# Kernel optimization log

Hardware: AMD Instinct MI355X
Metric: run time of the kernel (lower is better)

The kernel has to match this reference:

```python
import jax, jax.numpy as jnp
import numpy as np

N, T, IN, H, OUT, E = 50000, 12, 2, 128, 12, 800000


def setup_inputs() -> dict:
    key = jax.random.key(0)
    ks = jax.random.split(key, 20)
    s_in = 1.0 / np.sqrt(H)

    def w(k, shape):
        return jax.random.uniform(k, shape, jnp.float32, -s_in, s_in)

    return {
        "x": jax.random.normal(ks[0], (N, T, IN), jnp.float32),
        "edge_index": jax.random.randint(ks[1], (2, E), 0, N, dtype=jnp.int32),
        # LSTM layer 0 (input_dim -> H), gate order i,f,g,o as in PyTorch
        "Wih0": w(ks[2], (4 * H, IN)), "Whh0": w(ks[3], (4 * H, H)),
        "bih0": w(ks[4], (4 * H,)), "bhh0": w(ks[5], (4 * H,)),
        # LSTM layer 1 (H -> H)
        "Wih1": w(ks[6], (4 * H, H)), "Whh1": w(ks[7], (4 * H, H)),
        "bih1": w(ks[8], (4 * H,)), "bhh1": w(ks[9], (4 * H,)),
        # GCN layers
        "W0": w(ks[10], (H, H)), "b0": w(ks[11], (H,)),
        "W1": w(ks[12], (H, H)), "b1": w(ks[13], (H,)),
        "W2": w(ks[14], (H, OUT)), "b2": w(ks[15], (OUT,)),
    }


def _lstm_layer(seq, Wih, Whh, bih, bhh):
    # seq: [T, N, D] -> outputs [T, N, H]
    n = seq.shape[1]
    h0 = jnp.zeros((n, H), seq.dtype)
    c0 = jnp.zeros((n, H), seq.dtype)
    b = bih + bhh

    def step(carry, xt):
        h, c = carry
        z = xt @ Wih.T + h @ Whh.T + b
        i, f, g, o = jnp.split(z, 4, axis=-1)
        c = jax.nn.sigmoid(f) * c + jax.nn.sigmoid(i) * jnp.tanh(g)
        h = jax.nn.sigmoid(o) * jnp.tanh(c)
        return (h, c), h

    _, ys = jax.lax.scan(step, (h0, c0), seq)
    return ys


def _gcn(h, W, b, src, dst, norm):
    # x @ W, gather sources, edge-normalize, scatter-add to targets, + bias
    hW = h @ W
    msg = hW[src] * norm[:, None]
    return jax.ops.segment_sum(msg, dst, num_segments=N) + b


def reference(x, edge_index, Wih0, Whh0, bih0, bhh0, Wih1, Whh1, bih1, bhh1,
              W0, b0, W1, b1, W2, b2):
    # 2-layer LSTM over node time series (dropout inactive at inference)
    seq = jnp.transpose(x, (1, 0, 2))          # [T, N, IN]
    y0 = _lstm_layer(seq, Wih0, Whh0, bih0, bhh0)
    y1 = _lstm_layer(y0, Wih1, Whh1, bih1, bhh1)
    h = y1[-1]                                  # last timestep: [N, H]

    # GCN normalization with self-loops (symmetric, all edge weights 1)
    loops = jnp.arange(N, dtype=edge_index.dtype)
    src = jnp.concatenate([edge_index[0], loops])
    dst = jnp.concatenate([edge_index[1], loops])
    deg = jax.ops.segment_sum(jnp.ones(src.shape[0], h.dtype), dst, num_segments=N)
    dinv = jax.lax.rsqrt(deg)                   # deg >= 1 thanks to self-loops
    norm = dinv[src] * dinv[dst]

    h = jax.nn.relu(_gcn(h, W0, b0, src, dst, norm))
    h = jax.nn.relu(_gcn(h, W1, b1, src, dst, norm))
    out = _gcn(h, W2, b2, src, dst, norm)       # [N, OUT]
    return out
```

## Files before the change

### kernel.cpp

```cpp
#include <hip/hip_runtime.h>
#include <hip/hip_bf16.h>

#define TT 12
#define HDIM 128
#define ODIM 12
#define KS0 136
#define TPAD 36

typedef short bf16x8 __attribute__((ext_vector_type(8)));
typedef float f32x16 __attribute__((ext_vector_type(16)));
typedef float f32x4  __attribute__((ext_vector_type(4)));

__device__ __forceinline__ float fastrcp(float x) { return __builtin_amdgcn_rcpf(x); }
__device__ __forceinline__ float sigf(float x) { return fastrcp(1.f + __expf(-x)); }
__device__ __forceinline__ float tanh_fast(float x) { return 1.f - 2.f * fastrcp(1.f + __expf(2.f * x)); }
__device__ __forceinline__ unsigned short f2bf(float f) {
    union { float f; unsigned int u; } v; v.f = f;
    unsigned int r = v.u + 0x7FFFu + ((v.u >> 16) & 1u);
    return (unsigned short)(r >> 16);
}

__global__ void pack_kernel(const float* __restrict__ Whh0, const float* __restrict__ Wih1,
                            const float* __restrict__ Whh1, unsigned short* __restrict__ Wpk)
{
    int idx = blockIdx.x * 256 + threadIdx.x;
    if (idx >= 384 * 64) return;
    int lane = idx & 63;
    int slot = idx >> 6;
    int mat = slot >> 7;
    int rem = slot & 127;
    if (mat == 0) {
        int cb = rem >> 3, s = rem & 7;
        int col = cb * 32 + (lane & 31);
#pragma unroll
        for (int j = 0; j < 8; ++j) {
            int k = s * 16 + ((lane >> 5) << 3) + j;
            Wpk[((size_t)(slot * 64 + lane) << 3) + j] = f2bf(Whh0[col * 128 + k]);
        }
    } else {
        const float* src = (mat == 1) ? Wih1 : Whh1;
        int ct = rem >> 2, ks = rem & 3;
        int col = ct * 16 + (lane & 15);
#pragma unroll
        for (int j = 0; j < 8; ++j) {
            int k = ks * 32 + ((lane >> 4) << 3) + j;
            Wpk[((size_t)(slot * 64 + lane) << 3) + j] = f2bf(src[col * 128 + k]);
        }
    }
}

__global__ __launch_bounds__(512, 1) void lstm_l0_kernel(
    const float* __restrict__ x,
    const unsigned short* __restrict__ Wpk,
    const float* __restrict__ Wih0,
    const float* __restrict__ bih0, const float* __restrict__ bhh0,
    unsigned short* __restrict__ h0seq,
    int N, int ntiles)
{
    __shared__ unsigned short wlds[65536];
    __shared__ unsigned short hA0[64 * KS0];
    __shared__ float xls[64 * 24];

    const int tid  = threadIdx.x;
    const int w    = tid >> 6;
    const int ln   = tid & 63;
    const int ln31 = ln & 31;
    const int half = ln >> 5;
    const int wsub = w & 3;
    const int rb   = w >> 2;
    const int col  = wsub * 32 + ln31;

    for (int i = tid * 8; i < 65536; i += 512 * 8)
        *(bf16x8*)(wlds + i) = *(const bf16x8*)(Wpk + i);

    float wx0[4], wx1[4], br0[4];
#pragma unroll
    for (int g = 0; g < 4; ++g) {
        int row = (g << 7) + col;
        wx0[g] = Wih0[row * 2 + 0];
        wx1[g] = Wih0[row * 2 + 1];
        br0[g] = bih0[row] + bhh0[row];
    }

    for (int tile = blockIdx.x; tile < ntiles; tile += gridDim.x) {
        const int nbase = tile * 64;
        __syncthreads();
        for (int i = tid; i < 64 * 24; i += 512) {
            int n = nbase + i / 24;
            xls[i] = (n < N) ? x[nbase * 24 + i] : 0.f;
        }
        for (int i = tid; i < 64 * KS0; i += 512) hA0[i] = 0;
        float c0[16];
#pragma unroll
        for (int r = 0; r < 16; ++r) c0[r] = 0.f;
        __syncthreads();

        for (int t = 0; t < TT; ++t) {
            f32x16 acc[4];
#pragma unroll
            for (int g = 0; g < 4; ++g)
#pragma unroll
                for (int e = 0; e < 16; ++e) acc[g][e] = 0.f;
#pragma unroll
            for (int s = 0; s < 8; ++s) {
                bf16x8 a = *(const bf16x8*)(hA0 + (rb * 32 + ln31) * KS0 + s * 16 + half * 8);
#pragma unroll
                for (int g = 0; g < 4; ++g) {
                    int cb = g * 4 + wsub;
                    bf16x8 b = *(const bf16x8*)(wlds + (((cb * 8 + s) * 64 + ln) << 3));
                    acc[g] = __builtin_amdgcn_mfma_f32_32x32x16_bf16(a, b, acc[g], 0, 0, 0);
                }
            }
            __syncthreads();
#pragma unroll
            for (int r = 0; r < 16; ++r) {
                int node = rb * 32 + (r & 3) + 8 * (r >> 2) + 4 * half;
                float xa = xls[node * 24 + t * 2 + 0];
                float xb = xls[node * 24 + t * 2 + 1];
                float zi = acc[0][r] + br0[0] + wx0[0] * xa + wx1[0] * xb;
                float zf = acc[1][r] + br0[1] + wx0[1] * xa + wx1[1] * xb;
                float zg = acc[2][r] + br0[2] + wx0[2] * xa + wx1[2] * xb;
                float zo = acc[3][r] + br0[3] + wx0[3] * xa + wx1[3] * xb;
                float cn = sigf(zf) * c0[r] + sigf(zi) * tanh_fast(zg);
                c0[r] = cn;
                float h = sigf(zo) * tanh_fast(cn);
                unsigned short us = f2bf(h);
                hA0[node * KS0 + col] = us;
                int n = nbase + node;
                if (n < N) h0seq[(n * TT + t) * HDIM + col] = us;
            }
            __syncthreads();
        }
    }
}

__global__ __launch_bounds__(512) void lstm_l1f_kernel(
    const unsigned short* __restrict__ h0seq,
    const unsigned short* __restrict__ Wpk,
    const float* __restrict__ bih1, const float* __restrict__ bhh1,
    float* __restrict__ hbuf,
    int N, int ntiles)
{
    __shared__ unsigned short wlds[65536];
    __shared__ unsigned short hA1[64 * KS0];

    const int tid  = threadIdx.x;
    const int w    = tid >> 6;
    const int ln   = tid & 63;
    const int l15  = ln & 15;
    const int quad = ln >> 4;
    const int ch   = w * 16 + l15;

    for (int i = tid * 8; i < 65536; i += 512 * 8)
        *(bf16x8*)(wlds + i) = *(const bf16x8*)(Wpk + 131072 + i);

    bf16x8 wfr[4][4];
#pragma unroll
    for (int g = 0; g < 4; ++g)
#pragma unroll
        for (int ks = 0; ks < 4; ++ks) {
            int slot = (g * 8 + w) * 4 + ks;
            wfr[g][ks] = *(const bf16x8*)(Wpk + 65536 + ((size_t)(slot * 64 + ln) << 3));
        }

    float br1[4];
#pragma unroll
    for (int g = 0; g < 4; ++g) {
        int row = (g << 7) + ch;
        br1[g] = bih1[row] + bhh1[row];
    }

    const bf16x8 zv = {0, 0, 0, 0, 0, 0, 0, 0};
    __syncthreads();

    for (int tile = blockIdx.x; tile < ntiles; tile += gridDim.x) {
        __syncthreads();
        for (int i = tid; i < 64 * KS0; i += 512) hA1[i] = 0;
        float c1[16];
#pragma unroll
        for (int r = 0; r < 16; ++r) c1[r] = 0.f;
        __syncthreads();

        for (int t = 0; t < TT; ++t) {
            f32x4 acc[4][4];
#pragma unroll
            for (int rt = 0; rt < 4; ++rt)
#pragma unroll
                for (int g = 0; g < 4; ++g)
#pragma unroll
                    for (int e = 0; e < 4; ++e) acc[rt][g][e] = 0.f;

#pragma unroll
            for (int ks = 0; ks < 4; ++ks) {
                bf16x8 a[4];
#pragma unroll
                for (int rt = 0; rt < 4; ++rt) {
                    int n = tile * 64 + rt * 16 + l15;
                    a[rt] = (n < N)
                        ? __builtin_nontemporal_load(
                            (const bf16x8*)(h0seq + ((size_t)n * TT + t) * HDIM + ks * 32 + quad * 8))
                        : zv;
                }
#pragma unroll
                for (int g = 0; g < 4; ++g)
#pragma unroll
                    for (int rt = 0; rt < 4; ++rt)
                        acc[rt][g] = __builtin_amdgcn_mfma_f32_16x16x32_bf16(a[rt], wfr[g][ks], acc[rt][g], 0, 0, 0);
            }
#pragma unroll
            for (int ks = 0; ks < 4; ++ks) {
                bf16x8 a[4];
#pragma unroll
                for (int rt = 0; rt < 4; ++rt)
                    a[rt] = *(const bf16x8*)(hA1 + (rt * 16 + l15) * KS0 + ks * 32 + quad * 8);
#pragma unroll
                for (int g = 0; g < 4; ++g) {
                    int slot = (g * 8 + w) * 4 + ks;
                    bf16x8 b = *(const bf16x8*)(wlds + ((size_t)(slot * 64 + ln) << 3));
#pragma unroll
                    for (int rt = 0; rt < 4; ++rt)
                        acc[rt][g] = __builtin_amdgcn_mfma_f32_16x16x32_bf16(a[rt], b, acc[rt][g], 0, 0, 0);
                }
            }
            __syncthreads();

#pragma unroll
            for (int rt = 0; rt < 4; ++rt) {
#pragma unroll
                for (int rg = 0; rg < 4; ++rg) {
                    int ci = rt * 4 + rg;
                    float zi = acc[rt][0][rg] + br1[0];
                    float zf = acc[rt][1][rg] + br1[1];
                    float zg = acc[rt][2][rg] + br1[2];
                    float zo = acc[rt][3][rg] + br1[3];
                    float cn = sigf(zf) * c1[ci] + sigf(zi) * tanh_fast(zg);
                    c1[ci] = cn;
                    float h = sigf(zo) * tanh_fast(cn);
                    int nd = rt * 16 + quad * 4 + rg;
                    if (t + 1 < TT) {
                        hA1[nd * KS0 + ch] = f2bf(h);
                    } else {
                        int n = tile * 64 + nd;
                        if (n < N) hbuf[n * HDIM + ch] = h;
                    }
                }
            }
            __syncthreads();
        }
    }
}

__global__ void deg_count_kernel(const int* __restrict__ ei, int* __restrict__ degi, int E)
{
    int e = blockIdx.x * 256 + threadIdx.x;
    if (e < E) atomicAdd(&degi[ei[E + e]], 1);
}

__global__ void row_alloc_kernel(const int* __restrict__ degi, int* __restrict__ row_ptr,
                                 float* __restrict__ dinv, int* __restrict__ counter, int N)
{
    int n = blockIdx.x * 256 + threadIdx.x;
    int lane = threadIdx.x & 63;
    int v = (n < N) ? degi[n] : 0;
    int incl = v;
    for (int off = 1; off < 64; off <<= 1) {
        int u = __shfl_up(incl, off);
        if (lane >= off) incl += u;
    }
    int base = 0;
    if (lane == 63) base = atomicAdd(counter, incl);
    base = __shfl(base, 63);
    if (n < N) {
        row_ptr[n] = base + (incl - v);
        dinv[n] = rsqrtf((float)(v + 1));
    }
}

__global__ void csr_fill_kernel(const int* __restrict__ ei, const int* __restrict__ row_ptr,
                                int* __restrict__ fill, int* __restrict__ csr_src, int E)
{
    int e = blockIdx.x * 256 + threadIdx.x;
    if (e < E) {
        int d = ei[E + e];
        int p = atomicAdd(&fill[d], 1);
        csr_src[row_ptr[d] + p] = ei[e];
    }
}

__global__ __launch_bounds__(256) void gemm128_kernel(const float* __restrict__ X,
                                                      const float* __restrict__ W,
                                                      _Float16* __restrict__ Y, int N)
{
    __shared__ float XT[128 * TPAD];
    const int tid = threadIdx.x;
    const int nbase = blockIdx.x * 32;
    for (int idx = tid; idx < 32 * 128; idx += 256) {
        int m = idx >> 7, k = idx & 127;
        int n = nbase + m;
        XT[k * TPAD + m] = (n < N) ? X[n * HDIM + k] : 0.f;
    }
    __syncthreads();
    const int c  = tid & 63;
    const int mb = (tid >> 6) << 3;
    float acc[8][2];
#pragma unroll
    for (int i = 0; i < 8; ++i) { acc[i][0] = 0.f; acc[i][1] = 0.f; }
    for (int k = 0; k < 128; ++k) {
        const float* xr = &XT[k * TPAD + mb];
        float4 a0 = *(const float4*)(xr);
        float4 a1 = *(const float4*)(xr + 4);
        float a[8] = {a0.x, a0.y, a0.z, a0.w, a1.x, a1.y, a1.z, a1.w};
        float b0 = W[k * HDIM + c];
        float b1 = W[k * HDIM + c + 64];
#pragma unroll
        for (int i = 0; i < 8; ++i) {
            acc[i][0] = fmaf(a[i], b0, acc[i][0]);
            acc[i][1] = fmaf(a[i], b1, acc[i][1]);
        }
    }
#pragma unroll
    for (int i = 0; i < 8; ++i) {
        int n = nbase + mb + i;
        if (n < N) {
            Y[n * HDIM + c]      = (_Float16)acc[i][0];
            Y[n * HDIM + c + 64] = (_Float16)acc[i][1];
        }
    }
}

__global__ void gemm12_kernel(const float* __restrict__ X, const float* __restrict__ W2,
                              _Float16* __restrict__ Y, int N)
{
    int idx = blockIdx.x * 256 + threadIdx.x;
    int n = idx / ODIM, c = idx - n * ODIM;
    if (n >= N) return;
    float acc = 0.f;
    for (int k = 0; k < 128; ++k) acc = fmaf(X[n * HDIM + k], W2[k * ODIM + c], acc);
    Y[n * ODIM + c] = (_Float16)acc;
}

__global__ __launch_bounds__(128) void agg128_kernel(const _Float16* __restrict__ hW,
        const int* __restrict__ row_ptr, const int* __restrict__ degi,
        const int* __restrict__ csr_src, const float* __restrict__ dinv,
        const float* __restrict__ bias, float* __restrict__ out, int N, int do_relu)
{
    int n = blockIdx.x;
    int c = threadIdx.x;
    float dn = dinv[n];
    float acc = (float)hW[n * HDIM + c] * dn * dn;
    int start = row_ptr[n];
    int cnt = degi[n];
    for (int i = 0; i < cnt; ++i) {
        int s = csr_src[start + i];
        acc = fmaf((float)hW[s * HDIM + c], dinv[s] * dn, acc);
    }
    float v = acc + bias[c];
    if (do_relu) v = fmaxf(v, 0.f);
    out[n * HDIM + c] = v;
}

__global__ void agg12_kernel(const _Float16* __restrict__ hW, const int* __restrict__ row_ptr,
        const int* __restrict__ degi, const int* __restrict__ csr_src,
        const float* __restrict__ dinv, const float* __restrict__ b2,
        float* __restrict__ out, int N)
{
    int idx = blockIdx.x * 256 + threadIdx.x;
    int n = idx / ODIM, c = idx - n * ODIM;
    if (n >= N) return;
    float dn = dinv[n];
    float acc = (float)hW[n * ODIM + c] * dn * dn;
    int start = row_ptr[n], cnt = degi[n];
    for (int i = 0; i < cnt; ++i) {
        int s = csr_src[start + i];
        acc = fmaf((float)hW[s * ODIM + c], dinv[s] * dn, acc);
    }
    out[n * ODIM + c] = acc + b2[c];
}

extern "C" void kernel_launch(void* const* d_in, const int* in_sizes, int n_in,
                              void* d_out, int out_size, void* d_ws, size_t ws_size,
                              hipStream_t stream)
{
    const float* x     = (const float*)d_in[0];
    const int*   ei    = (const int*)d_in[1];
    const float* Wih0  = (const float*)d_in[2];
    const float* Whh0  = (const float*)d_in[3];
    const float* bih0  = (const float*)d_in[4];
    const float* bhh0  = (const float*)d_in[5];
    const float* Wih1  = (const float*)d_in[6];
    const float* Whh1  = (const float*)d_in[7];
    const float* bih1  = (const float*)d_in[8];
    const float* bhh1  = (const float*)d_in[9];
    const float* W0    = (const float*)d_in[10];
    const float* b0    = (const float*)d_in[11];
    const float* W1    = (const float*)d_in[12];
    const float* b1    = (const float*)d_in[13];
    const float* W2    = (const float*)d_in[14];
    const float* b2    = (const float*)d_in[15];
    float* out = (float*)d_out;

    const int N = in_sizes[0] / (TT * 2);
    const int E = in_sizes[1] / 2;

    unsigned short* Wpk = (unsigned short*)d_ws;
    float* fbase = (float*)((char*)d_ws + 393216);
    float* hbuf = fbase;
    float* buf1 = hbuf + (size_t)N * HDIM;
    float* buf2 = buf1 + (size_t)N * HDIM;
    float* dinv = buf2 + (size_t)N * HDIM;
    int* degi    = (int*)(dinv + N);
    int* fill    = degi + N;
    int* counter = fill + N;
    int* row_ptr = counter + 1;
    int* csr_src = row_ptr + N;
    size_t h0_off = (((size_t)((char*)(csr_src + E) - (char*)d_ws)) + 255) & ~(size_t)255;
    unsigned short* h0seq = (unsigned short*)((char*)d_ws + h0_off);
    _Float16* buf1h = (_Float16*)buf1;

    hipMemsetAsync(degi, 0, (size_t)(2 * N + 1) * sizeof(int), stream);

    pack_kernel<<<(384 * 64 + 255) / 256, 256, 0, stream>>>(Whh0, Wih1, Whh1, Wpk);

    const int ntiles = (N + 63) / 64;
    lstm_l0_kernel<<<256, 512, 0, stream>>>(x, Wpk, Wih0, bih0, bhh0, h0seq, N, ntiles);
    lstm_l1f_kernel<<<256, 512, 0, stream>>>(h0seq, Wpk, bih1, bhh1, hbuf, N, ntiles);

    deg_count_kernel<<<(E + 255) / 256, 256, 0, stream>>>(ei, degi, E);
    row_alloc_kernel<<<(N + 255) / 256, 256, 0, stream>>>(degi, row_ptr, dinv, counter, N);
    csr_fill_kernel<<<(E + 255) / 256, 256, 0, stream>>>(ei, row_ptr, fill, csr_src, E);

    gemm128_kernel<<<(N + 31) / 32, 256, 0, stream>>>(hbuf, W0, buf1h, N);
    agg128_kernel<<<N, 128, 0, stream>>>(buf1h, row_ptr, degi, csr_src, dinv, b0, buf2, N, 1);
    gemm128_kernel<<<(N + 31) / 32, 256, 0, stream>>>(buf2, W1, buf1h, N);
    agg128_kernel<<<N, 128, 0, stream>>>(buf1h, row_ptr, degi, csr_src, dinv, b1, buf2, N, 1);
    gemm12_kernel<<<((size_t)N * ODIM + 255) / 256, 256, 0, stream>>>(buf2, W2, buf1h, N);
    agg12_kernel<<<((size_t)N * ODIM + 255) / 256, 256, 0, stream>>>(
        buf1h, row_ptr, degi, csr_src, dinv, b2, out, N);
}
```

Baseline: 1.068 ms.

## Double-buffer LSTM layer-1 hidden state and prefetch next-step inputs into registers

In the layer-1 LSTM kernel the shared hidden-state buffer becomes two buffers that alternate per timestep, which removes one block barrier per step. The next timestep's layer-0 outputs are loaded from global memory into registers while the current step's MFMAs run. The LDS layout changes to a fragment-ordered format so each lane reads contiguous 16-byte chunks without padding. This holds 16 more bf16x8 registers per thread, which may increase register pressure and reduce occupancy.

```diff
diff --git a/kernel.cpp b/kernel.cpp
--- a/kernel.cpp
+++ b/kernel.cpp
@@ -142,7 +142,7 @@
     int N, int ntiles)
 {
     __shared__ unsigned short wlds[65536];
-    __shared__ unsigned short hA1[64 * KS0];
+    __shared__ unsigned short hA1[2][8192];
 
     const int tid  = threadIdx.x;
     const int w    = tid >> 6;
@@ -150,6 +150,9 @@
     const int l15  = ln & 15;
     const int quad = ln >> 4;
     const int ch   = w * 16 + l15;
+    const int chk  = ch >> 5;
+    const int chq  = (ch >> 3) & 3;
+    const int chj  = ch & 7;
 
     for (int i = tid * 8; i < 65536; i += 512 * 8)
         *(bf16x8*)(wlds + i) = *(const bf16x8*)(Wpk + 131072 + i);
@@ -175,13 +178,36 @@
 
     for (int tile = blockIdx.x; tile < ntiles; tile += gridDim.x) {
         __syncthreads();
-        for (int i = tid; i < 64 * KS0; i += 512) hA1[i] = 0;
+        for (int i = tid; i < 1024; i += 512)
+            *(bf16x8*)(hA1[0] + i * 8) = zv;
         float c1[16];
 #pragma unroll
         for (int r = 0; r < 16; ++r) c1[r] = 0.f;
+
+        int na[4]; bool ok[4];
+#pragma unroll
+        for (int rt = 0; rt < 4; ++rt) { na[rt] = tile * 64 + rt * 16 + l15; ok[rt] = na[rt] < N; }
+
+        bf16x8 aA[8], aB[8];
+#pragma unroll
+        for (int ks = 0; ks < 2; ++ks)
+#pragma unroll
+            for (int rt = 0; rt < 4; ++rt)
+                aA[ks * 4 + rt] = ok[rt] ? __builtin_nontemporal_load(
+                    (const bf16x8*)(h0seq + ((size_t)na[rt] * TT + 0) * HDIM + ks * 32 + quad * 8)) : zv;
+#pragma unroll
+        for (int ks = 0; ks < 2; ++ks)
+#pragma unroll
+            for (int rt = 0; rt < 4; ++rt)
+                aB[ks * 4 + rt] = ok[rt] ? __builtin_nontemporal_load(
+                    (const bf16x8*)(h0seq + ((size_t)na[rt] * TT + 0) * HDIM + (ks + 2) * 32 + quad * 8)) : zv;
         __syncthreads();
 
         for (int t = 0; t < TT; ++t) {
+            const unsigned short* usp = hA1[t & 1];
+            unsigned short* dst = hA1[(t & 1) ^ 1];
+            const bool pf = (t + 1 < TT);
+
             f32x4 acc[4][4];
 #pragma unroll
             for (int rt = 0; rt < 4; ++rt)
@@ -189,30 +215,41 @@
                 for (int g = 0; g < 4; ++g)
 #pragma unroll
                     for (int e = 0; e < 4; ++e) acc[rt][g][e] = 0.f;
+
+#pragma unroll
+            for (int ks = 0; ks < 2; ++ks)
+#pragma unroll
+                for (int g = 0; g < 4; ++g)
+#pragma unroll
+                    for (int rt = 0; rt < 4; ++rt)
+                        acc[rt][g] = __builtin_amdgcn_mfma_f32_16x16x32_bf16(aA[ks * 4 + rt], wfr[g][ks], acc[rt][g], 0, 0, 0);
+#pragma unroll
+            for (int ks = 0; ks < 2; ++ks)
+#pragma unroll
+                for (int rt = 0; rt < 4; ++rt)
+                    aA[ks * 4 + rt] = (pf && ok[rt]) ? __builtin_nontemporal_load(
+                        (const bf16x8*)(h0seq + ((size_t)na[rt] * TT + t + 1) * HDIM + ks * 32 + quad * 8)) : aA[ks * 4 + rt];
+
+#pragma unroll
+            for (int ks = 0; ks < 2; ++ks)
+#pragma unroll
+                for (int g = 0; g < 4; ++g)
+#pragma unroll
+                    for (int rt = 0; rt < 4; ++rt)
+                        acc[rt][g] = __builtin_amdgcn_mfma_f32_16x16x32_bf16(aB[ks * 4 + rt], wfr[g][ks + 2], acc[rt][g], 0, 0, 0);
+#pragma unroll
+            for (int ks = 0; ks < 2; ++ks)
+#pragma unroll
+                for (int rt = 0; rt < 4; ++rt)
+                    aB[ks * 4 + rt] = (pf && ok[rt]) ? __builtin_nontemporal_load(
+                        (const bf16x8*)(h0seq + ((size_t)na[rt] * TT + t + 1) * HDIM + (ks + 2) * 32 + quad * 8)) : aB[ks * 4 + rt];
 
 #pragma unroll
             for (int ks = 0; ks < 4; ++ks) {
                 bf16x8 a[4];
 #pragma unroll
-                for (int rt = 0; rt < 4; ++rt) {
-                    int n = tile * 64 + rt * 16 + l15;
-                    a[rt] = (n < N)
-                        ? __builtin_nontemporal_load(
-                            (const bf16x8*)(h0seq + ((size_t)n * TT + t) * HDIM + ks * 32 + quad * 8))
-                        : zv;
-                }
-#pragma unroll
-                for (int g = 0; g < 4; ++g)
-#pragma unroll
-                    for (int rt = 0; rt < 4; ++rt)
-                        acc[rt][g] = __builtin_amdgcn_mfma_f32_16x16x32_bf16(a[rt], wfr[g][ks], acc[rt][g], 0, 0, 0);
-            }
-#pragma unroll
-            for (int ks = 0; ks < 4; ++ks) {
-                bf16x8 a[4];
-#pragma unroll
                 for (int rt = 0; rt < 4; ++rt)
-                    a[rt] = *(const bf16x8*)(hA1 + (rt * 16 + l15) * KS0 + ks * 32 + quad * 8);
+                    a[rt] = *(const bf16x8*)(usp + (((rt * 4 + ks) * 64 + ln) << 3));
 #pragma unroll
                 for (int g = 0; g < 4; ++g) {
                     int slot = (g * 8 + w) * 4 + ks;
@@ -222,7 +259,6 @@
                         acc[rt][g] = __builtin_amdgcn_mfma_f32_16x16x32_bf16(a[rt], b, acc[rt][g], 0, 0, 0);
                 }
             }
-            __syncthreads();
 
 #pragma unroll
             for (int rt = 0; rt < 4; ++rt) {
@@ -236,11 +272,10 @@
                     float cn = sigf(zf) * c1[ci] + sigf(zi) * tanh_fast(zg);
                     c1[ci] = cn;
                     float h = sigf(zo) * tanh_fast(cn);
-                    int nd = rt * 16 + quad * 4 + rg;
                     if (t + 1 < TT) {
-                        hA1[nd * KS0 + ch] = f2bf(h);
+                        dst[(((rt * 4 + chk) * 64 + chq * 16 + quad * 4 + rg) << 3) + chj] = f2bf(h);
                     } else {
-                        int n = tile * 64 + nd;
+                        int n = tile * 64 + rt * 16 + quad * 4 + rg;
                         if (n < N) hbuf[n * HDIM + ch] = h;
                     }
                 }
```

New measurement: 1.103 ms. +3.2%, slower.

## Coalesce layer-0 h0seq stores and double-buffer layer-1 hidden state in fragment layout

Applied to the files above, without the earlier changes.

Layer-0 LSTM now writes h0seq through LDS with 16-byte per-thread stores after the step barrier, replacing scattered 2-byte global stores. Layer-1 keeps its recurrent hidden state in two LDS buffers laid out in MFMA fragment order, which removes one barrier per timestep and the padded-row reads. It also replaces the nontemporal h0seq loads with plain loads and precomputes node bounds. The trade-off is an extra LDS read pass in layer 0 and more LDS use in layer 1.

```diff
diff --git a/kernel.cpp b/kernel.cpp
--- a/kernel.cpp
+++ b/kernel.cpp
@@ -69,6 +69,8 @@
     const int wsub = w & 3;
     const int rb   = w >> 2;
     const int col  = wsub * 32 + ln31;
+    const int cm   = tid >> 3;
+    const int cc0  = (tid & 7) << 4;
 
     for (int i = tid * 8; i < 65536; i += 512 * 8)
         *(bf16x8*)(wlds + i) = *(const bf16x8*)(Wpk + i);
@@ -94,6 +96,9 @@
 #pragma unroll
         for (int r = 0; r < 16; ++r) c0[r] = 0.f;
         __syncthreads();
+
+        const int ncp = nbase + cm;
+        const bool cok = ncp < N;
 
         for (int t = 0; t < TT; ++t) {
             f32x16 acc[4];
@@ -124,12 +129,16 @@
                 float cn = sigf(zf) * c0[r] + sigf(zi) * tanh_fast(zg);
                 c0[r] = cn;
                 float h = sigf(zo) * tanh_fast(cn);
-                unsigned short us = f2bf(h);
-                hA0[node * KS0 + col] = us;
-                int n = nbase + node;
-                if (n < N) h0seq[(n * TT + t) * HDIM + col] = us;
+                hA0[node * KS0 + col] = f2bf(h);
             }
             __syncthreads();
+            if (cok) {
+                bf16x8 v0 = *(const bf16x8*)(hA0 + cm * KS0 + cc0);
+                bf16x8 v1 = *(const bf16x8*)(hA0 + cm * KS0 + cc0 + 8);
+                unsigned short* dp = h0seq + ((size_t)ncp * TT + t) * HDIM + cc0;
+                *(bf16x8*)(dp)     = v0;
+                *(bf16x8*)(dp + 8) = v1;
+            }
         }
     }
 }
@@ -142,7 +151,7 @@
     int N, int ntiles)
 {
     __shared__ unsigned short wlds[65536];
-    __shared__ unsigned short hA1[64 * KS0];
+    __shared__ unsigned short hA1[2][8192];
 
     const int tid  = threadIdx.x;
     const int w    = tid >> 6;
@@ -150,6 +159,9 @@
     const int l15  = ln & 15;
     const int quad = ln >> 4;
     const int ch   = w * 16 + l15;
+    const int chk  = ch >> 5;
+    const int chq  = (ch >> 3) & 3;
+    const int chj  = ch & 7;
 
     for (int i = tid * 8; i < 65536; i += 512 * 8)
         *(bf16x8*)(wlds + i) = *(const bf16x8*)(Wpk + 131072 + i);
@@ -175,13 +187,21 @@
 
     for (int tile = blockIdx.x; tile < ntiles; tile += gridDim.x) {
         __syncthreads();
-        for (int i = tid; i < 64 * KS0; i += 512) hA1[i] = 0;
+        for (int i = tid; i < 1024; i += 512)
+            *(bf16x8*)(hA1[0] + i * 8) = zv;
         float c1[16];
 #pragma unroll
         for (int r = 0; r < 16; ++r) c1[r] = 0.f;
+
+        int na[4]; bool ok[4];
+#pragma unroll
+        for (int rt = 0; rt < 4; ++rt) { na[rt] = tile * 64 + rt * 16 + l15; ok[rt] = na[rt] < N; }
         __syncthreads();
 
         for (int t = 0; t < TT; ++t) {
+            const unsigned short* usp = hA1[t & 1];
+            unsigned short* dst = hA1[(t & 1) ^ 1];
+
             f32x4 acc[4][4];
 #pragma unroll
             for (int rt = 0; rt < 4; ++rt)
@@ -194,13 +214,10 @@
             for (int ks = 0; ks < 4; ++ks) {
                 bf16x8 a[4];
 #pragma unroll
-                for (int rt = 0; rt < 4; ++rt) {
-                    int n = tile * 64 + rt * 16 + l15;
-                    a[rt] = (n < N)
-                        ? __builtin_nontemporal_load(
-                            (const bf16x8*)(h0seq + ((size_t)n * TT + t) * HDIM + ks * 32 + quad * 8))
+                for (int rt = 0; rt < 4; ++rt)
+                    a[rt] = ok[rt]
+                        ? *(const bf16x8*)(h0seq + ((size_t)na[rt] * TT + t) * HDIM + ks * 32 + quad * 8)
                         : zv;
-                }
 #pragma unroll
                 for (int g = 0; g < 4; ++g)
 #pragma unroll
@@ -212,7 +229,7 @@
                 bf16x8 a[4];
 #pragma unroll
                 for (int rt = 0; rt < 4; ++rt)
-                    a[rt] = *(const bf16x8*)(hA1 + (rt * 16 + l15) * KS0 + ks * 32 + quad * 8);
+                    a[rt] = *(const bf16x8*)(usp + (((rt * 4 + ks) * 64 + ln) << 3));
 #pragma unroll
                 for (int g = 0; g < 4; ++g) {
                     int slot = (g * 8 + w) * 4 + ks;
@@ -222,7 +239,6 @@
                         acc[rt][g] = __builtin_amdgcn_mfma_f32_16x16x32_bf16(a[rt], b, acc[rt][g], 0, 0, 0);
                 }
             }
-            __syncthreads();
 
 #pragma unroll
             for (int rt = 0; rt < 4; ++rt) {
@@ -236,11 +252,10 @@
                     float cn = sigf(zf) * c1[ci] + sigf(zi) * tanh_fast(zg);
                     c1[ci] = cn;
                     float h = sigf(zo) * tanh_fast(cn);
-                    int nd = rt * 16 + quad * 4 + rg;
                     if (t + 1 < TT) {
-                        hA1[nd * KS0 + ch] = f2bf(h);
+                        dst[(((rt * 4 + chk) * 64 + chq * 16 + quad * 4 + rg) << 3) + chj] = f2bf(h);
                     } else {
-                        int n = tile * 64 + nd;
+                        int n = tile * 64 + rt * 16 + quad * 4 + rg;
                         if (n < N) hbuf[n * HDIM + ch] = h;
                     }
                 }
```

Result: faster. 1.037 ms (-3.0%).
